# Kernel tuning notes

Hardware: AMD Instinct MI355X
Metric: run time of the kernel (lower is better)

Reference implementation:

```python
import jax, jax.numpy as jnp
import numpy as np

TEMP = 0.07
W00 = 0.1
EPS = 1e-8


def setup_inputs() -> dict:
    key = jax.random.key(0)
    k1, k2, k3, k4 = jax.random.split(key, 4)
    B, N, D = 32, 256, 256
    M = B * N
    return {
        "audio_feats": jax.random.normal(k1, (B, N, D), dtype=jnp.float32),
        "visual_feats": jax.random.normal(k2, (B, N, D), dtype=jnp.float32),
        "audio_labels": jax.random.randint(k3, (M,), 0, 2, dtype=jnp.int64)
            if jax.config.jax_enable_x64 else jax.random.randint(k3, (M,), 0, 2, dtype=jnp.int32),
        "visual_labels": jax.random.randint(k4, (M,), 0, 2, dtype=jnp.int64)
            if jax.config.jax_enable_x64 else jax.random.randint(k4, (M,), 0, 2, dtype=jnp.int32),
    }


def reference(audio_feats, visual_feats, audio_labels, visual_labels):
    B, N, D = audio_feats.shape
    M = B * N
    a = audio_feats.reshape(M, D)
    v = visual_feats.reshape(M, D)
    # L2 normalize (torch F.normalize uses eps=1e-12 clamp on norm)
    a = a / jnp.maximum(jnp.linalg.norm(a, axis=-1, keepdims=True), 1e-12)
    v = v / jnp.maximum(jnp.linalg.norm(v, axis=-1, keepdims=True), 1e-12)
    sim = (a @ v.T) / TEMP  # (M, M)
    exp_sim = jnp.exp(sim)
    la = audio_labels[:, None]  # (M, 1)
    lv = visual_labels[None, :]  # (1, M)
    pos_mask = (la == lv) & ((la == 1) | (la == 0))
    weight = jnp.where(la == 1, 1.0, W00) * pos_mask.astype(sim.dtype)  # (M, M)
    wexp = exp_sim * weight

    # audio -> visual (row direction)
    denom_a2v = exp_sim.sum(axis=1)
    num_a2v = wexp.sum(axis=1)
    frac_a2v = (num_a2v + EPS) / (denom_a2v + EPS)
    valid_a2v = (num_a2v > 0).astype(sim.dtype)
    loss_a2v = -(valid_a2v * jnp.log(frac_a2v)).sum() / jnp.maximum(valid_a2v.sum(), 1.0)

    # visual -> audio (column direction)
    denom_v2a = exp_sim.sum(axis=0)
    num_v2a = wexp.sum(axis=0)
    frac_v2a = (num_v2a + EPS) / (denom_v2a + EPS)
    valid_v2a = (num_v2a > 0).astype(sim.dtype)
    loss_v2a = -(valid_v2a * jnp.log(frac_v2a)).sum() / jnp.maximum(valid_v2a.sum(), 1.0)

    return 0.5 * (loss_a2v + loss_v2a)
```

## Files before the change

kernel.cpp:

```cpp
#include <hip/hip_runtime.h>

#define M_ROWS 8192
#define D_DIM  256
#define BM     256
#define BN     128
#define BK     64
#define NBI    (M_ROWS / BM)
#define NBJ    (M_ROWS / BN)

#define ALPHA  4.53982478f

typedef __attribute__((ext_vector_type(8))) short  short8;
typedef __attribute__((ext_vector_type(4))) float  floatx4;

__device__ inline unsigned short f2bf(float f) {
    union { float f; unsigned int u; } v; v.f = f;
    unsigned int u = v.u;
    u = (u + 0x7fffu + ((u >> 16) & 1u)) >> 16;
    return (unsigned short)u;
}

__device__ inline float fast_exp2(float x) {
#if __has_builtin(__builtin_amdgcn_exp2f)
    return __builtin_amdgcn_exp2f(x);
#else
    return exp2f(x);
#endif
}

__device__ inline void async_copy16(const void* gptr, void* lptr) {
    __builtin_amdgcn_global_load_lds(
        (const __attribute__((address_space(1))) unsigned int*)gptr,
        (__attribute__((address_space(3))) unsigned int*)lptr,
        16, 0, 0);
}

__global__ void normalize_kernel(const float* __restrict__ af, const float* __restrict__ vf,
                                 unsigned short* __restrict__ aB, unsigned short* __restrict__ vB)
{
    const int wave = threadIdx.x >> 6, lane = threadIdx.x & 63;
    int row = blockIdx.x * 4 + wave;
    const float* src;
    unsigned short* dst;
    if (row < M_ROWS) { src = af + (size_t)row * D_DIM;            dst = aB + (size_t)row * D_DIM; }
    else              { src = vf + (size_t)(row - M_ROWS) * D_DIM; dst = vB + (size_t)(row - M_ROWS) * D_DIM; }
    float4 x = *(const float4*)(src + lane * 4);
    float ss = x.x*x.x + x.y*x.y + x.z*x.z + x.w*x.w;
    #pragma unroll
    for (int m = 1; m < 64; m <<= 1) ss += __shfl_xor(ss, m, 64);
    float scale = ALPHA / fmaxf(sqrtf(ss), 1e-12f);
    ushort4 o;
    o.x = f2bf(x.x * scale); o.y = f2bf(x.y * scale);
    o.z = f2bf(x.z * scale); o.w = f2bf(x.w * scale);
    *(ushort4*)(dst + lane * 4) = o;
}

__global__ __launch_bounds__(256, 2) void gemm_loss_kernel(
    const unsigned short* __restrict__ aB, const unsigned short* __restrict__ vB,
    const int* __restrict__ la, const int* __restrict__ lv,
    float* __restrict__ rowPart, float* __restrict__ colPart)
{
    __shared__ unsigned short lA[BM * BK];
    __shared__ unsigned short lV[BN * BK];

    const int tid  = threadIdx.x;
    const int wave = tid >> 6, lane = tid & 63;
    const int quad = lane >> 4, l16 = lane & 15;

    const int super = blockIdx.x >> 8;
    const int inner = blockIdx.x & 255;
    const int bx = (super & 1) * 16 + (inner & 15);
    const int by = (super >> 1) * 16 + (inner >> 4);
    const int i0 = bx * BM, j0 = by * BN;

    const int drow = lane >> 3;
    const int dg   = (lane & 7) ^ drow;
    const unsigned short* gA0 = aB + (size_t)(i0 + drow) * D_DIM + dg * 8;
    const unsigned short* gV0 = vB + (size_t)(j0 + drow) * D_DIM + dg * 8;

    floatx4 acc[4][8] = {};

    #pragma unroll
    for (int ks = 0; ks < D_DIM / BK; ++ks) {
        __syncthreads();
        #pragma unroll
        for (int t = 0; t < 8; ++t) {
            const int slot = wave * 8 + t;
            async_copy16(gA0 + (size_t)slot * 8 * D_DIM + ks * BK, lA + slot * 512);
        }
        #pragma unroll
        for (int t = 0; t < 4; ++t) {
            const int slot = wave * 4 + t;
            async_copy16(gV0 + (size_t)slot * 8 * D_DIM + ks * BK, lV + slot * 512);
        }
        __syncthreads();
        #pragma unroll
        for (int kk = 0; kk < 2; ++kk) {
            const int pc = ((kk * 4 + quad) ^ (l16 & 7)) * 8;
            short8 afr[4], bfr[8];
            #pragma unroll
            for (int it = 0; it < 4; ++it)
                afr[it] = *(const short8*)&lA[(wave * 64 + it * 16 + l16) * BK + pc];
            #pragma unroll
            for (int jt = 0; jt < 8; ++jt)
                bfr[jt] = *(const short8*)&lV[(jt * 16 + l16) * BK + pc];
            #pragma unroll
            for (int it = 0; it < 4; ++it)
                #pragma unroll
                for (int jt = 0; jt < 8; ++jt)
                    acc[it][jt] = __builtin_amdgcn_mfma_f32_16x16x32_bf16(
                        afr[it], bfr[jt], acc[it][jt], 0, 0, 0);
        }
    }

    const int baseRow = i0 + wave * 64;
    float maf[4][4];
    #pragma unroll
    for (int it = 0; it < 4; ++it)
        #pragma unroll
        for (int r = 0; r < 4; ++r)
            maf[it][r] = (float)la[baseRow + it * 16 + quad * 4 + r];
    float mvf[8];
    #pragma unroll
    for (int jt = 0; jt < 8; ++jt)
        mvf[jt] = (float)lv[j0 + jt * 16 + l16];

    float rT[4][4] = {}, r1[4][4] = {};
    float cT[8] = {}, c1[8] = {};
    #pragma unroll
    for (int it = 0; it < 4; ++it) {
        #pragma unroll
        for (int jt = 0; jt < 8; ++jt) {
            #pragma unroll
            for (int r = 0; r < 4; ++r) {
                float e = fast_exp2(acc[it][jt][r]);
                rT[it][r] += e;
                r1[it][r] = fmaf(mvf[jt], e, r1[it][r]);
                cT[jt] += e;
                c1[jt] = fmaf(maf[it][r], e, c1[jt]);
            }
        }
    }

    #pragma unroll
    for (int jt = 0; jt < 8; ++jt) {
        float t0 = cT[jt], t1 = c1[jt];
        t0 += __shfl_xor(t0, 16, 64); t0 += __shfl_xor(t0, 32, 64);
        t1 += __shfl_xor(t1, 16, 64); t1 += __shfl_xor(t1, 32, 64);
        cT[jt] = t0; c1[jt] = t1;
    }

    __syncthreads();
    float* rowbuf = (float*)lA;
    float* colbuf = (float*)lA + 512;

    #pragma unroll
    for (int it = 0; it < 4; ++it) {
        #pragma unroll
        for (int r = 0; r < 4; ++r) {
            float s0 = rT[it][r], s1 = r1[it][r];
            #pragma unroll
            for (int m = 1; m < 16; m <<= 1) {
                s0 += __shfl_xor(s0, m, 64);
                s1 += __shfl_xor(s1, m, 64);
            }
            if (l16 == 0) {
                int rl = wave * 64 + it * 16 + quad * 4 + r;
                rowbuf[rl * 2 + 0] = s0;
                rowbuf[rl * 2 + 1] = s1;
            }
        }
    }
    if (quad == 0) {
        #pragma unroll
        for (int jt = 0; jt < 8; ++jt) {
            colbuf[(wave * 2 + 0) * BN + jt * 16 + l16] = cT[jt];
            colbuf[(wave * 2 + 1) * BN + jt * 16 + l16] = c1[jt];
        }
    }
    __syncthreads();

    {
        *(float2*)&rowPart[((size_t)by * M_ROWS + i0 + tid) * 2] = ((float2*)rowbuf)[tid];
        const int rl  = tid >> 1;
        const int cls = tid & 1;
        float s = colbuf[(0 * 2 + cls) * BN + rl] + colbuf[(1 * 2 + cls) * BN + rl]
                + colbuf[(2 * 2 + cls) * BN + rl] + colbuf[(3 * 2 + cls) * BN + rl];
        colPart[((size_t)bx * M_ROWS + j0 + rl) * 2 + cls] = s;
    }
}

__global__ __launch_bounds__(256) void reduce_kernel(
    const float* __restrict__ rowPart, const float* __restrict__ colPart,
    const int* __restrict__ la, const int* __restrict__ lv,
    float* __restrict__ blockPart)
{
    const int bid = blockIdx.x;
    const bool aside = bid < 32;
    const int idx = (aside ? bid : bid - 32) * 256 + threadIdx.x;
    const float* part = aside ? rowPart : colPart;
    const int* lab = aside ? la : lv;
    const int nb = aside ? NBJ : NBI;

    float tot = 0.f, c1 = 0.f;
    #pragma unroll 4
    for (int b = 0; b < nb; ++b) {
        float2 p = *(const float2*)(part + ((size_t)b * M_ROWS + idx) * 2);
        tot += p.x; c1 += p.y;
    }
    float num = lab[idx] ? c1 : 0.1f * (tot - c1);
    float lg = 0.f, cnt = 0.f;
    if (num > 0.f) { lg = logf((num + 1e-8f) / (tot + 1e-8f)); cnt = 1.f; }

    #pragma unroll
    for (int m = 1; m < 64; m <<= 1) {
        lg  += __shfl_xor(lg,  m, 64);
        cnt += __shfl_xor(cnt, m, 64);
    }
    __shared__ float red[4][2];
    const int w = threadIdx.x >> 6, ln = threadIdx.x & 63;
    if (ln == 0) { red[w][0] = lg; red[w][1] = cnt; }
    __syncthreads();
    if (threadIdx.x == 0) {
        blockPart[bid * 2 + 0] = red[0][0] + red[1][0] + red[2][0] + red[3][0];
        blockPart[bid * 2 + 1] = red[0][1] + red[1][1] + red[2][1] + red[3][1];
    }
}

__global__ void finalize_kernel(const float* __restrict__ blockPart, float* __restrict__ out)
{
    const int lane = threadIdx.x & 63;
    float lg  = blockPart[lane * 2 + 0];
    float cnt = blockPart[lane * 2 + 1];
    #pragma unroll
    for (int m = 1; m < 32; m <<= 1) {
        lg  += __shfl_xor(lg,  m, 64);
        cnt += __shfl_xor(cnt, m, 64);
    }
    float sA = __shfl(lg, 0, 64),  cA = __shfl(cnt, 0, 64);
    float sV = __shfl(lg, 32, 64), cV = __shfl(cnt, 32, 64);
    if (threadIdx.x == 0) {
        float lossA = -sA / fmaxf(cA, 1.f);
        float lossV = -sV / fmaxf(cV, 1.f);
        out[0] = 0.5f * (lossA + lossV);
    }
}

extern "C" void kernel_launch(void* const* d_in, const int* in_sizes, int n_in,
                              void* d_out, int out_size, void* d_ws, size_t ws_size,
                              hipStream_t stream)
{
    const float* af = (const float*)d_in[0];
    const float* vf = (const float*)d_in[1];
    const int*   la = (const int*)d_in[2];
    const int*   lv = (const int*)d_in[3];
    float* out = (float*)d_out;

    char* ws = (char*)d_ws;
    unsigned short* aB = (unsigned short*)ws;
    unsigned short* vB = (unsigned short*)(ws + 4ull * 1024 * 1024);
    float* rowPart   = (float*)(ws +  8ull * 1024 * 1024);
    float* colPart   = (float*)(ws + 12ull * 1024 * 1024);
    float* blockPart = (float*)(ws + 14ull * 1024 * 1024);

    normalize_kernel<<<(2 * M_ROWS) / 4, 256, 0, stream>>>(af, vf, aB, vB);
    gemm_loss_kernel<<<NBI * NBJ, 256, 0, stream>>>(aB, vB, la, lv, rowPart, colPart);
    reduce_kernel<<<64, 256, 0, stream>>>(rowPart, colPart, la, lv, blockPart);
    finalize_kernel<<<1, 64, 0, stream>>>(blockPart, out);
}
```

Before: 136.3 us.

## Load MFMA operands directly from global memory with register double-buffering instead of LDS

Removes the LDS staging (global_load_lds async copies plus two barriers per K step) and has each wave load its A and V bf16 fragments straight from global memory into registers, double-buffered across 32-wide K steps. The aim is to drop the synchronization and LDS traffic in the main loop. The cost is that the V tile is loaded redundantly by all four waves and accesses are 16-byte strided row reads, which leans on L1/L2 caching. It also raises register pressure under launch_bounds(256,2). The epilogue buffers become dedicated shared arrays and the barrier before them is removed.

```diff
diff --git a/kernel.cpp b/kernel.cpp
--- a/kernel.cpp
+++ b/kernel.cpp
@@ -4,7 +4,6 @@
 #define D_DIM  256
 #define BM     256
 #define BN     128
-#define BK     64
 #define NBI    (M_ROWS / BM)
 #define NBJ    (M_ROWS / BN)
 
@@ -26,13 +25,6 @@
 #else
     return exp2f(x);
 #endif
-}
-
-__device__ inline void async_copy16(const void* gptr, void* lptr) {
-    __builtin_amdgcn_global_load_lds(
-        (const __attribute__((address_space(1))) unsigned int*)gptr,
-        (__attribute__((address_space(3))) unsigned int*)lptr,
-        16, 0, 0);
 }
 
 __global__ void normalize_kernel(const float* __restrict__ af, const float* __restrict__ vf,
@@ -60,9 +52,6 @@
     const int* __restrict__ la, const int* __restrict__ lv,
     float* __restrict__ rowPart, float* __restrict__ colPart)
 {
-    __shared__ unsigned short lA[BM * BK];
-    __shared__ unsigned short lV[BN * BK];
-
     const int tid  = threadIdx.x;
     const int wave = tid >> 6, lane = tid & 63;
     const int quad = lane >> 4, l16 = lane & 15;
@@ -73,44 +62,35 @@
     const int by = (super >> 1) * 16 + (inner >> 4);
     const int i0 = bx * BM, j0 = by * BN;
 
-    const int drow = lane >> 3;
-    const int dg   = (lane & 7) ^ drow;
-    const unsigned short* gA0 = aB + (size_t)(i0 + drow) * D_DIM + dg * 8;
-    const unsigned short* gV0 = vB + (size_t)(j0 + drow) * D_DIM + dg * 8;
+    const unsigned short* Ab = aB + (size_t)(i0 + wave * 64 + l16) * D_DIM + quad * 8;
+    const unsigned short* Vb = vB + (size_t)(j0 + l16) * D_DIM + quad * 8;
 
     floatx4 acc[4][8] = {};
-
-    #pragma unroll
-    for (int ks = 0; ks < D_DIM / BK; ++ks) {
-        __syncthreads();
-        #pragma unroll
-        for (int t = 0; t < 8; ++t) {
-            const int slot = wave * 8 + t;
-            async_copy16(gA0 + (size_t)slot * 8 * D_DIM + ks * BK, lA + slot * 512);
-        }
-        #pragma unroll
-        for (int t = 0; t < 4; ++t) {
-            const int slot = wave * 4 + t;
-            async_copy16(gV0 + (size_t)slot * 8 * D_DIM + ks * BK, lV + slot * 512);
-        }
-        __syncthreads();
-        #pragma unroll
-        for (int kk = 0; kk < 2; ++kk) {
-            const int pc = ((kk * 4 + quad) ^ (l16 & 7)) * 8;
-            short8 afr[4], bfr[8];
+    short8 afr[2][4], bfr[2][8];
+
+    #pragma unroll
+    for (int it = 0; it < 4; ++it) afr[0][it] = *(const short8*)(Ab + it * 16 * D_DIM);
+    #pragma unroll
+    for (int jt = 0; jt < 8; ++jt) bfr[0][jt] = *(const short8*)(Vb + jt * 16 * D_DIM);
+
+    #pragma unroll
+    for (int k32 = 0; k32 < 8; ++k32) {
+        const int cur = k32 & 1, nxt = cur ^ 1;
+        if (k32 < 7) {
+            const int ko = (k32 + 1) * 32;
             #pragma unroll
             for (int it = 0; it < 4; ++it)
-                afr[it] = *(const short8*)&lA[(wave * 64 + it * 16 + l16) * BK + pc];
+                afr[nxt][it] = *(const short8*)(Ab + it * 16 * D_DIM + ko);
             #pragma unroll
             for (int jt = 0; jt < 8; ++jt)
-                bfr[jt] = *(const short8*)&lV[(jt * 16 + l16) * BK + pc];
-            #pragma unroll
-            for (int it = 0; it < 4; ++it)
-                #pragma unroll
-                for (int jt = 0; jt < 8; ++jt)
-                    acc[it][jt] = __builtin_amdgcn_mfma_f32_16x16x32_bf16(
-                        afr[it], bfr[jt], acc[it][jt], 0, 0, 0);
-        }
+                bfr[nxt][jt] = *(const short8*)(Vb + jt * 16 * D_DIM + ko);
+        }
+        #pragma unroll
+        for (int it = 0; it < 4; ++it)
+            #pragma unroll
+            for (int jt = 0; jt < 8; ++jt)
+                acc[it][jt] = __builtin_amdgcn_mfma_f32_16x16x32_bf16(
+                    afr[cur][it], bfr[cur][jt], acc[it][jt], 0, 0, 0);
     }
 
     const int baseRow = i0 + wave * 64;
@@ -150,9 +130,8 @@
         cT[jt] = t0; c1[jt] = t1;
     }
 
-    __syncthreads();
-    float* rowbuf = (float*)lA;
-    float* colbuf = (float*)lA + 512;
+    __shared__ float rowbuf[2 * BM];
+    __shared__ float colbuf[8 * BN];
 
     #pragma unroll
     for (int it = 0; it < 4; ++it) {
```

New measurement: 188.7 us. 1.38x slower.
